# Optimization experiments

Hardware: AMD Instinct MI355X
Metric: run time of the kernel (lower is better)

Reference implementation:

```python
import jax, jax.numpy as jnp
import numpy as np

T, D, H, KEXP = 91, 256, 4, 4
DH = D // H
NA, NRG = 128, 1024
NEG = -1e10
SCALE = 2.0  # sqrt(head_num=4), faithful to the original (NOT sqrt(dh))


def _ln(x, g, b, eps=1e-5):
    m = jnp.mean(x, axis=-1, keepdims=True)
    v = jnp.mean((x - m) ** 2, axis=-1, keepdims=True)
    return (x - m) * jax.lax.rsqrt(v + eps) * g + b


def setup_inputs() -> dict:
    key = jax.random.key(0)
    ks = jax.random.split(key, 16)
    s = lambda fan_in: 1.0 / np.sqrt(fan_in)
    inp = {
        "agent": jax.random.normal(ks[0], (NA, T, D), jnp.float32),
        "rg": jax.random.normal(ks[1], (NRG, T, D), jnp.float32),
        "ln_x_g": jnp.ones((D,), jnp.float32),
        "ln_x_b": jnp.zeros((D,), jnp.float32),
        "wk": jax.random.uniform(ks[2], (D, D), jnp.float32, -s(D), s(D)),
        "bk": jnp.zeros((D,), jnp.float32),
        "wv": jax.random.uniform(ks[3], (D, D), jnp.float32, -s(D), s(D)),
        "bv": jnp.zeros((D,), jnp.float32),
        "wq": jax.random.uniform(ks[4], (D, D), jnp.float32, -s(D), s(D)),
        "bq": jnp.zeros((D,), jnp.float32),
        "q_scale": jnp.full((DH,), 0.001, jnp.float32),
        "wy": jax.random.uniform(ks[5], (D, D), jnp.float32, -s(D), s(D)),
        "by": jnp.zeros((D,), jnp.float32),
        "wf1": jax.random.uniform(ks[6], (D, KEXP * D), jnp.float32, -s(D), s(D)),
        "bf1": jnp.zeros((KEXP * D,), jnp.float32),
        "wf2": jax.random.uniform(ks[7], (KEXP * D, D), jnp.float32, -s(KEXP * D), s(KEXP * D)),
        "bf2": jnp.zeros((D,), jnp.float32),
        "ln_z_g": jnp.ones((D,), jnp.float32),
        "ln_z_b": jnp.zeros((D,), jnp.float32),
        "agent_rg_mask": jax.random.randint(ks[8], (T, NA, NRG), 0, 2).astype(bool),
        "padding_mask": jax.random.randint(ks[9], (T, NRG), 0, 2).astype(bool),
        "rg_valid_mask": jax.random.randint(ks[10], (T, NA), 0, 2).astype(bool),
    }
    return inp


def reference(agent, rg, ln_x_g, ln_x_b, wk, bk, wv, bv, wq, bq, q_scale,
              wy, by, wf1, bf1, wf2, bf2, ln_z_g, ln_z_b,
              agent_rg_mask, padding_mask, rg_valid_mask):
    agent_n = _ln(agent, ln_x_g, ln_x_b)   # (Na, T, D)
    rg_n = _ln(rg, ln_x_g, ln_x_b)         # (Nrg, T, D)

    K = jax.nn.relu(rg_n @ wk + bk).reshape(NRG, T, H, DH)
    V = jax.nn.relu(rg_n @ wv + bv).reshape(NRG, T, H, DH)
    Q = jax.nn.relu(agent_n @ wq + bq).reshape(NA, T, H, DH) * q_scale

    # energy: (T, H, Na, Nrg)
    energy = jnp.einsum("athd,rthd->thar", Q, K) / SCALE
    energy = jnp.where(agent_rg_mask[:, None, :, :], energy, NEG)
    energy = jnp.where(padding_mask[:, None, None, :], energy, NEG)
    energy = jnp.where(rg_valid_mask[:, None, :, None], energy, NEG)
    attn = jax.nn.softmax(energy, axis=-1)

    Y1 = jnp.einsum("thar,rthd->athd", attn, V).reshape(NA, T, D)
    Y2 = jax.nn.relu(Y1 @ wy + by)
    S = Y2 + agent_n
    F1 = jax.nn.relu(S @ wf1 + bf1)
    F2 = jax.nn.relu(F1 @ wf2 + bf2)
    Z = _ln(F2, ln_z_g, ln_z_b)

    Qp = jnp.transpose(Q, (1, 2, 0, 3))  # (T,H,Na,dh)
    Kp = jnp.transpose(K, (1, 2, 0, 3))
    Vp = jnp.transpose(V, (1, 2, 0, 3))
    return (Z, Qp, Kp, Vp)
```

## Files before the change

### kernel.cpp

```cpp
#include <hip/hip_runtime.h>

#define T_   91
#define D_   256
#define H_   4
#define DH_  64
#define NA_  128
#define NRG_ 1024
#define KEXP_ 4

typedef float f32x4 __attribute__((ext_vector_type(4)));
typedef short bf16x8 __attribute__((ext_vector_type(8)));

static constexpr float P_EPS = 1.3877787807814457e-17f;

__device__ inline ushort f2bf(float f) {
    union { float f; unsigned u; } v; v.f = f;
    unsigned r = (v.u + 0x7fffu + ((v.u >> 16) & 1u)) >> 16;
    return (ushort)r;
}
__device__ inline unsigned pk2(float a, float b) {
    return (unsigned)f2bf(a) | ((unsigned)f2bf(b) << 16);
}
__device__ inline float bf2f(ushort b) {
    union { unsigned u; float f; } v; v.u = ((unsigned)b) << 16;
    return v.f;
}

#define LN_BLOCKS 2912
#define PM_BLOCKS 2912
#define PW_BLOCKS 3072

__global__ __launch_bounds__(256) void prep_all(
    const float* __restrict__ agent,
    const float* __restrict__ g, const float* __restrict__ b,
    const int* __restrict__ am, const int* __restrict__ pm,
    const int* __restrict__ vmk,
    const float* __restrict__ wk, const float* __restrict__ wv,
    const float* __restrict__ wq, const float* __restrict__ wy,
    const float* __restrict__ wf1, const float* __restrict__ wf2,
    ushort* __restrict__ agn, unsigned* __restrict__ cm,
    ushort* __restrict__ wkvt, ushort* __restrict__ wqt,
    ushort* __restrict__ wyt, ushort* __restrict__ wf1t,
    ushort* __restrict__ wf2t) {
    __shared__ int pmS[NRG_];
    int bid = blockIdx.x;
    if (bid < LN_BLOCKS) {
        int row = bid * 4 + (threadIdx.x >> 6);
        int lane = threadIdx.x & 63;
        f32x4 x = *(const f32x4*)(agent + (size_t)row * D_ + lane * 4);
        float s1 = x[0] + x[1] + x[2] + x[3];
        float s2 = x[0] * x[0] + x[1] * x[1] + x[2] * x[2] + x[3] * x[3];
#pragma unroll
        for (int off = 1; off < 64; off <<= 1) {
            s1 += __shfl_xor(s1, off);
            s2 += __shfl_xor(s2, off);
        }
        float mean = s1 * (1.0f / 256.0f);
        float var = s2 * (1.0f / 256.0f) - mean * mean;
        float rstd = rsqrtf(var + 1e-5f);
        f32x4 gv = *(const f32x4*)(g + lane * 4);
        f32x4 bv = *(const f32x4*)(b + lane * 4);
        float y0 = (x[0] - mean) * rstd * gv[0] + bv[0];
        float y1 = (x[1] - mean) * rstd * gv[1] + bv[1];
        float y2 = (x[2] - mean) * rstd * gv[2] + bv[2];
        float y3 = (x[3] - mean) * rstd * gv[3] + bv[3];
        *(uint2*)(agn + (size_t)row * D_ + lane * 4) =
            make_uint2(pk2(y0, y1), pk2(y2, y3));
    } else if (bid < LN_BLOCKS + PM_BLOCKS) {
        int base = (bid - LN_BLOCKS) * 4;
        int t = base / NA_;
        int w = threadIdx.x >> 6, lane = threadIdx.x & 63;
#pragma unroll
        for (int i = 0; i < 4; ++i)
            pmS[threadIdx.x + i * 256] = pm[(size_t)t * NRG_ + threadIdx.x + i * 256];
        __syncthreads();
        int idx = base + w;
        int a = idx & (NA_ - 1);
        int valid = vmk[t * NA_ + a];
        const int* amrow = am + (size_t)idx * NRG_;
#pragma unroll
        for (int c = 0; c < 16; ++c) {
            int r = c * 64 + lane;
            bool bit = valid && amrow[r] && pmS[r];
            unsigned long long msk = __ballot(bit);
            if (lane == 0) {
                cm[(size_t)idx * 32 + c * 2]     = (unsigned)msk;
                cm[(size_t)idx * 32 + c * 2 + 1] = (unsigned)(msk >> 32);
            }
        }
    } else {
        int idx = (bid - LN_BLOCKS - PM_BLOCKS) * 256 + threadIdx.x;
        if (idx < 131072) {
            const float* W = (idx < 65536) ? wk : wv;
            int li = idx & 65535;
            int n = li >> 8, k = li & 255;
            wkvt[idx] = f2bf(W[(size_t)k * 256 + n]);
        } else if (idx < 196608) {
            int li = idx - 131072;
            int n = li >> 8, k = li & 255;
            wqt[li] = f2bf(wq[(size_t)k * 256 + n]);
        } else if (idx < 262144) {
            int li = idx - 196608;
            int n = li >> 8, k = li & 255;
            wyt[li] = f2bf(wy[(size_t)k * 256 + n]);
        } else if (idx < 524288) {
            int li = idx - 262144;
            int n = li >> 8, k = li & 255;
            wf1t[li] = f2bf(wf1[(size_t)k * 1024 + n]);
        } else {
            int li = idx - 524288;
            int n = li >> 10, k = li & 1023;
            wf2t[li] = f2bf(wf2[(size_t)k * 256 + n]);
        }
    }
}

__global__ __launch_bounds__(512) void gemm_kvq(
    const float* __restrict__ rgf, const ushort* __restrict__ agn,
    const float* __restrict__ lng, const float* __restrict__ lnb,
    const ushort* __restrict__ wkvt, const ushort* __restrict__ wqt,
    const float* __restrict__ bk, const float* __restrict__ bv,
    const float* __restrict__ bq, const float* __restrict__ qs,
    float* __restrict__ Kp, float* __restrict__ Vp, float* __restrict__ Qp,
    ushort* __restrict__ Kb, ushort* __restrict__ Vtb, ushort* __restrict__ Qb) {
    __shared__ ushort Asf[64][264];
    __shared__ ushort Bs[256][72];
    float (*Et)[68] = (float(*)[68])&Asf[0][0];

    int bid = blockIdx.x;
    bool isQ = bid >= 2912;
    int bxi = 0, t, rb = 0, a0 = 0, bn = 0;
    if (!isQ) {
        int sub = bid & 15, pid = bid >> 4;
        bxi = sub >> 3;
        int by = pid * 8 + (sub & 7);
        t = by >> 4; rb = (by & 15) << 6;
        bn = bxi << 8;
    } else {
        int qid = bid - 2912;
        t = qid >> 1; a0 = (qid & 1) << 6;
    }
    const ushort* Bt = isQ ? wqt : wkvt;

    int tid = threadIdx.x;
    int w = tid >> 6, lane = tid & 63;
    int wm = w >> 2, wn = w & 3;
    int l15 = lane & 15, l4 = lane >> 4;

    if (!isQ) {
        int row = tid >> 3, l8 = tid & 7;
        const float* ap = rgf + ((size_t)(rb + row) * T_ + t) * 256;
        f32x4 xr[8];
#pragma unroll
        for (int c = 0; c < 8; ++c) xr[c] = *(const f32x4*)(ap + l8 * 4 + c * 32);
        float s1 = 0.0f, s2 = 0.0f;
#pragma unroll
        for (int c = 0; c < 8; ++c)
#pragma unroll
            for (int r = 0; r < 4; ++r) { s1 += xr[c][r]; s2 += xr[c][r] * xr[c][r]; }
#pragma unroll
        for (int off = 1; off < 8; off <<= 1) {
            s1 += __shfl_xor(s1, off);
            s2 += __shfl_xor(s2, off);
        }
        float mean = s1 * (1.0f / 256.0f);
        float var = s2 * (1.0f / 256.0f) - mean * mean;
        float rstd = rsqrtf(var + 1e-5f);
#pragma unroll
        for (int c = 0; c < 8; ++c) {
            int col = l8 * 4 + c * 32;
            f32x4 g4 = *(const f32x4*)(lng + col);
            f32x4 b4 = *(const f32x4*)(lnb + col);
            float y0 = (xr[c][0] - mean) * rstd * g4[0] + b4[0];
            float y1 = (xr[c][1] - mean) * rstd * g4[1] + b4[1];
            float y2 = (xr[c][2] - mean) * rstd * g4[2] + b4[2];
            float y3 = (xr[c][3] - mean) * rstd * g4[3] + b4[3];
            *(uint2*)&Asf[row][col] = make_uint2(pk2(y0, y1), pk2(y2, y3));
        }
    } else {
#pragma unroll
        for (int i2 = 0; i2 < 4; ++i2) {
            int chunk = tid + i2 * 512;
            int row = chunk >> 5, c8 = (chunk & 31) * 8;
            *(bf16x8*)&Asf[row][c8] =
                *(const bf16x8*)(agn + ((size_t)(a0 + row) * T_ + t) * 256 + c8);
        }
    }

    f32x4 acc[2][4];
#pragma unroll
    for (int i = 0; i < 2; ++i)
#pragma unroll
        for (int j = 0; j < 4; ++j)
#pragma unroll
            for (int r = 0; r < 4; ++r) acc[i][j][r] = 0.0f;

    for (int k0 = 0; k0 < 256; k0 += 64) {
#pragma unroll
        for (int it = 0; it < 4; ++it) {
            int li = tid + it * 512;
            int row = li >> 3, c8 = (li & 7) * 8;
            *(bf16x8*)&Bs[row][c8] =
                *(const bf16x8*)(Bt + (size_t)(bn + row) * 256 + k0 + c8);
        }
        __syncthreads();
#pragma unroll
        for (int kk = 0; kk < 2; ++kk) {
            bf16x8 af[2], bfr[4];
#pragma unroll
            for (int i = 0; i < 2; ++i)
                af[i] = *(const bf16x8*)&Asf[wm * 32 + i * 16 + l15][k0 + kk * 32 + l4 * 8];
#pragma unroll
            for (int j = 0; j < 4; ++j)
                bfr[j] = *(const bf16x8*)&Bs[wn * 64 + j * 16 + l15][kk * 32 + l4 * 8];
#pragma unroll
            for (int i = 0; i < 2; ++i)
#pragma unroll
                for (int j = 0; j < 4; ++j)
                    acc[i][j] = __builtin_amdgcn_mfma_f32_16x16x32_bf16(
                        af[i], bfr[j], acc[i][j], 0, 0, 0);
        }
        __syncthreads();
    }

    float v[2][4][4];
#pragma unroll
    for (int i = 0; i < 2; ++i)
#pragma unroll
        for (int j = 0; j < 4; ++j)
#pragma unroll
            for (int reg = 0; reg < 4; ++reg) {
                int nl = wn * 64 + j * 16 + l15;
                float bs = isQ ? bq[nl] : (bxi ? bv[nl] : bk[nl]);
                float x = fmaxf(acc[i][j][reg] + bs, 0.0f);
                if (isQ) x *= qs[nl & 63];
                v[i][j][reg] = x;
            }

#pragma unroll 1
    for (int jq = 0; jq < 4; ++jq) {
        __syncthreads();
        if (wn == jq) {
#pragma unroll
            for (int i = 0; i < 2; ++i)
#pragma unroll
                for (int j = 0; j < 4; ++j)
#pragma unroll
                    for (int reg = 0; reg < 4; ++reg)
                        Et[wm * 32 + i * 16 + l4 * 4 + reg][j * 16 + l15] = v[i][j][reg];
        }
        __syncthreads();

        if (isQ) {
            size_t base = (((size_t)t * H_ + jq) * NA_ + a0) * DH_;
#pragma unroll
            for (int it = 0; it < 2; ++it) {
                int slot = it * 512 + tid;
                int row = slot >> 4, c4 = (slot & 15) * 4;
                *(f32x4*)(Qp + base + row * 64 + c4) = *(f32x4*)&Et[row][c4];
                uint2 u = make_uint2(pk2(Et[row][c4] * 0.5f, Et[row][c4 + 1] * 0.5f),
                                     pk2(Et[row][c4 + 2] * 0.5f, Et[row][c4 + 3] * 0.5f));
                *(uint2*)(Qb + base + row * 64 + c4) = u;
            }
        } else {
            size_t base = (((size_t)t * H_ + jq) * NRG_ + rb) * DH_;
            float* of = bxi ? Vp : Kp;
#pragma unroll
            for (int it = 0; it < 2; ++it) {
                int slot = it * 512 + tid;
                int row = slot >> 4, c4 = (slot & 15) * 4;
                *(f32x4*)(of + base + row * 64 + c4) = *(f32x4*)&Et[row][c4];
            }
            if (!bxi) {
#pragma unroll
                for (int it = 0; it < 2; ++it) {
                    int slot = it * 512 + tid;
                    int row = slot >> 4, c4 = (slot & 15) * 4;
                    uint2 u = make_uint2(pk2(Et[row][c4], Et[row][c4 + 1]),
                                         pk2(Et[row][c4 + 2], Et[row][c4 + 3]));
                    *(uint2*)(Kb + base + row * 64 + c4) = u;
                }
            } else {
                __syncthreads();
                if (wn == jq) {
#pragma unroll
                    for (int i = 0; i < 2; ++i)
#pragma unroll
                        for (int j = 0; j < 4; ++j)
#pragma unroll
                            for (int reg = 0; reg < 4; ++reg)
                                Et[j * 16 + l15][wm * 32 + i * 16 + l4 * 4 + reg] = v[i][j][reg];
                }
                __syncthreads();
                size_t tb = ((size_t)t * H_ + jq) * DH_ * NRG_;
#pragma unroll
                for (int it = 0; it < 2; ++it) {
                    int slot = it * 512 + tid;
                    int d = slot >> 4, r4 = (slot & 15) * 4;
                    uint2 u = make_uint2(pk2(Et[d][r4], Et[d][r4 + 1]),
                                         pk2(Et[d][r4 + 2], Et[d][r4 + 3]));
                    *(uint2*)(Vtb + tb + (size_t)d * NRG_ + rb + r4) = u;
                }
            }
        }
    }
}

__global__ __launch_bounds__(512) void gemm_wide(
    const ushort* __restrict__ Ab, const ushort* __restrict__ Bt,
    const float* __restrict__ bias0, const float* __restrict__ bias1,
    const float* __restrict__ aux0, const ushort* __restrict__ residb,
    float* __restrict__ out0, ushort* __restrict__ out2,
    int N, int K, int mode) {
    __shared__ ushort smem[64 * 72 + 256 * 72];
    __shared__ float lnp[2][64][4];
    ushort (*As)[72] = (ushort(*)[72])smem;
    ushort (*Bs)[72] = (ushort(*)[72])(smem + 64 * 72);
    float (*Et)[68] = (float(*)[68])smem;

    int bxi = blockIdx.x, by = blockIdx.y;
    int bn = bxi * 256, bm = by * 64;

    int tid = threadIdx.x;
    int w = tid >> 6, lane = tid & 63;
    int wm = w >> 2, wn = w & 3;
    int l15 = lane & 15, l4 = lane >> 4;

    f32x4 acc[2][4];
#pragma unroll
    for (int i = 0; i < 2; ++i)
#pragma unroll
        for (int j = 0; j < 4; ++j)
#pragma unroll
            for (int r = 0; r < 4; ++r) acc[i][j][r] = 0.0f;

    for (int k0 = 0; k0 < K; k0 += 64) {
        {
            int row = tid >> 3, c8 = (tid & 7) * 8;
            *(bf16x8*)&As[row][c8] =
                *(const bf16x8*)(Ab + (size_t)(bm + row) * K + k0 + c8);
        }
#pragma unroll
        for (int it = 0; it < 4; ++it) {
            int li = tid + it * 512;
            int row = li >> 3, c8 = (li & 7) * 8;
            *(bf16x8*)&Bs[row][c8] =
                *(const bf16x8*)(Bt + (size_t)(bn + row) * K + k0 + c8);
        }
        __syncthreads();
#pragma unroll
        for (int kk = 0; kk < 2; ++kk) {
            bf16x8 af[2], bfr[4];
#pragma unroll
            for (int i = 0; i < 2; ++i)
                af[i] = *(const bf16x8*)&As[wm * 32 + i * 16 + l15][kk * 32 + l4 * 8];
#pragma unroll
            for (int j = 0; j < 4; ++j)
                bfr[j] = *(const bf16x8*)&Bs[wn * 64 + j * 16 + l15][kk * 32 + l4 * 8];
#pragma unroll
            for (int i = 0; i < 2; ++i)
#pragma unroll
                for (int j = 0; j < 4; ++j)
                    acc[i][j] = __builtin_amdgcn_mfma_f32_16x16x32_bf16(
                        af[i], bfr[j], acc[i][j], 0, 0, 0);
        }
        __syncthreads();
    }

    float v[2][4][4];
#pragma unroll
    for (int i = 0; i < 2; ++i)
#pragma unroll
        for (int j = 0; j < 4; ++j)
#pragma unroll
            for (int reg = 0; reg < 4; ++reg) {
                int nl = wn * 64 + j * 16 + l15;
                int rowl = wm * 32 + i * 16 + l4 * 4 + reg;
                float bs = (mode == 0) ? bias0[bn + nl] : bias0[nl];
                float x = fmaxf(acc[i][j][reg] + bs, 0.0f);
                if (mode == 3) x += bf2f(residb[(size_t)(bm + rowl) * 256 + nl]);
                v[i][j][reg] = x;
            }

    if (mode == 5) {
        float rs_[2][4], rq_[2][4];
#pragma unroll
        for (int i = 0; i < 2; ++i)
#pragma unroll
            for (int reg = 0; reg < 4; ++reg) {
                float s = 0.0f, q = 0.0f;
#pragma unroll
                for (int j = 0; j < 4; ++j) {
                    float x = v[i][j][reg];
                    s += x; q += x * x;
                }
#pragma unroll
                for (int off = 1; off < 16; off <<= 1) {
                    s += __shfl_xor(s, off);
                    q += __shfl_xor(q, off);
                }
                rs_[i][reg] = s; rq_[i][reg] = q;
            }
        if (l15 == 0) {
#pragma unroll
            for (int i = 0; i < 2; ++i)
#pragma unroll
                for (int reg = 0; reg < 4; ++reg) {
                    int row = wm * 32 + i * 16 + l4 * 4 + reg;
                    lnp[0][row][wn] = rs_[i][reg];
                    lnp[1][row][wn] = rq_[i][reg];
                }
        }
        __syncthreads();
#pragma unroll
        for (int i = 0; i < 2; ++i)
#pragma unroll
            for (int reg = 0; reg < 4; ++reg) {
                int row = wm * 32 + i * 16 + l4 * 4 + reg;
                float S1 = lnp[0][row][0] + lnp[0][row][1] + lnp[0][row][2] + lnp[0][row][3];
                float S2 = lnp[1][row][0] + lnp[1][row][1] + lnp[1][row][2] + lnp[1][row][3];
                float mean = S1 * (1.0f / 256.0f);
                float var = S2 * (1.0f / 256.0f) - mean * mean;
                float rstd = rsqrtf(var + 1e-5f);
#pragma unroll
                for (int j = 0; j < 4; ++j) {
                    int nl = wn * 64 + j * 16 + l15;
                    float z = (v[i][j][reg] - mean) * rstd * bias1[nl] + aux0[nl];
                    out0[(size_t)(bm + row) * 256 + nl] = z;
                }
            }
        return;
    }

#pragma unroll 1
    for (int jq = 0; jq < 4; ++jq) {
        __syncthreads();
        if (wn == jq) {
#pragma unroll
            for (int i = 0; i < 2; ++i)
#pragma unroll
                for (int j = 0; j < 4; ++j)
#pragma unroll
                    for (int reg = 0; reg < 4; ++reg)
                        Et[wm * 32 + i * 16 + l4 * 4 + reg][j * 16 + l15] = v[i][j][reg];
        }
        __syncthreads();
#pragma unroll
        for (int it = 0; it < 2; ++it) {
            int slot = it * 512 + tid;
            int row = slot >> 4, c4 = (slot & 15) * 4;
            uint2 u = make_uint2(pk2(Et[row][c4], Et[row][c4 + 1]),
                                 pk2(Et[row][c4 + 2], Et[row][c4 + 3]));
            *(uint2*)(out2 + (size_t)(bm + row) * N + bn + jq * 64 + c4) = u;
        }
    }
}

__global__ __launch_bounds__(512) void attn_flash(
    const ushort* __restrict__ Qb, const ushort* __restrict__ Kb,
    const ushort* __restrict__ Vtb, const unsigned* __restrict__ cm,
    ushort* __restrict__ Y1b) {
    int th = blockIdx.x;
    int t = th >> 2, h = th & 3;
    int tid = threadIdx.x;
    int w = tid >> 6, lane = tid & 63;
    int l15 = lane & 15, l4 = lane >> 4;

    __shared__ ushort Ks[2][64][72];
    __shared__ ushort Vts[2][64][72];
    __shared__ ushort Ps[128][72];
    __shared__ unsigned cmAll[128][33];

    bf16x8 qf[2];
#pragma unroll
    for (int kk = 0; kk < 2; ++kk)
        qf[kk] = *(const bf16x8*)(Qb + ((size_t)th * NA_ + w * 16 + l15) * DH_
                                  + kk * 32 + l4 * 8);

    {
        const uint4* src = (const uint4*)(cm + (size_t)t * NA_ * 32 + tid * 8);
        uint4 c0 = src[0], c1 = src[1];
        int a = tid >> 2, wd = (tid & 3) * 8;
        cmAll[a][wd + 0] = c0.x; cmAll[a][wd + 1] = c0.y;
        cmAll[a][wd + 2] = c0.z; cmAll[a][wd + 3] = c0.w;
        cmAll[a][wd + 4] = c1.x; cmAll[a][wd + 5] = c1.y;
        cmAll[a][wd + 6] = c1.z; cmAll[a][wd + 7] = c1.w;
    }

    int srow = tid >> 3, sc8 = (tid & 7) * 8;
    const ushort* Kbase = Kb + (size_t)th * NRG_ * DH_;
    const ushort* Vbase = Vtb + (size_t)th * DH_ * NRG_;
    bf16x8 kreg = *(const bf16x8*)(Kbase + (size_t)srow * DH_ + sc8);
    bf16x8 vreg = *(const bf16x8*)(Vbase + (size_t)srow * NRG_ + sc8);
    *(bf16x8*)&Ks[0][srow][sc8] = kreg;
    *(bf16x8*)&Vts[0][srow][sc8] = vreg;
    __syncthreads();

    f32x4 o[4];
    float rsum[4] = {0.0f, 0.0f, 0.0f, 0.0f};
#pragma unroll
    for (int ds = 0; ds < 4; ++ds)
#pragma unroll
        for (int r = 0; r < 4; ++r) o[ds][r] = 0.0f;

    for (int rt = 0; rt < 16; ++rt) {
        int cur = rt & 1;
        if (rt < 15) {
            int r0n = (rt + 1) * 64;
            kreg = *(const bf16x8*)(Kbase + (size_t)(r0n + srow) * DH_ + sc8);
            vreg = *(const bf16x8*)(Vbase + (size_t)srow * NRG_ + r0n + sc8);
        }

        f32x4 e[4];
#pragma unroll
        for (int rs = 0; rs < 4; ++rs) {
#pragma unroll
            for (int r = 0; r < 4; ++r) e[rs][r] = 0.0f;
#pragma unroll
            for (int kk = 0; kk < 2; ++kk) {
                bf16x8 kf = *(const bf16x8*)&Ks[cur][rs * 16 + l15][kk * 32 + l4 * 8];
                e[rs] = __builtin_amdgcn_mfma_f32_16x16x32_bf16(qf[kk], kf, e[rs], 0, 0, 0);
            }
        }

#pragma unroll
        for (int reg = 0; reg < 4; ++reg) {
            int a_loc = w * 16 + l4 * 4 + reg;
            unsigned w0 = cmAll[a_loc][rt * 2], w1 = cmAll[a_loc][rt * 2 + 1];
#pragma unroll
            for (int rs = 0; rs < 4; ++rs) {
                unsigned wd = (rs & 2) ? w1 : w0;
                int bit = (wd >> ((rs & 1) * 16 + l15)) & 1;
                float p = bit ? __expf(e[rs][reg]) : P_EPS;
                rsum[reg] += p;
                Ps[a_loc][rs * 16 + l15] = f2bf(p);
            }
        }

#pragma unroll
        for (int rc = 0; rc < 2; ++rc) {
            bf16x8 pa = *(const bf16x8*)&Ps[w * 16 + l15][rc * 32 + l4 * 8];
#pragma unroll
            for (int ds = 0; ds < 4; ++ds) {
                bf16x8 vf = *(const bf16x8*)&Vts[cur][ds * 16 + l15][rc * 32 + l4 * 8];
                o[ds] = __builtin_amdgcn_mfma_f32_16x16x32_bf16(pa, vf, o[ds], 0, 0, 0);
            }
        }

        if (rt < 15) {
            *(bf16x8*)&Ks[cur ^ 1][srow][sc8] = kreg;
            *(bf16x8*)&Vts[cur ^ 1][srow][sc8] = vreg;
            __syncthreads();
        }
    }

#pragma unroll
    for (int off = 1; off < 16; off <<= 1)
#pragma unroll
        for (int reg = 0; reg < 4; ++reg)
            rsum[reg] += __shfl_xor(rsum[reg], off);
    float rinv[4];
#pragma unroll
    for (int reg = 0; reg < 4; ++reg) rinv[reg] = 1.0f / rsum[reg];

#pragma unroll
    for (int ds = 0; ds < 4; ++ds)
#pragma unroll
        for (int reg = 0; reg < 4; ++reg) {
            int a_g = w * 16 + l4 * 4 + reg;
            int d = ds * 16 + l15;
            Y1b[((size_t)a_g * T_ + t) * D_ + h * DH_ + d] = f2bf(o[ds][reg] * rinv[reg]);
        }
}

extern "C" void kernel_launch(void* const* d_in, const int* in_sizes, int n_in,
                              void* d_out, int out_size, void* d_ws, size_t ws_size,
                              hipStream_t stream) {
    const float* agent   = (const float*)d_in[0];
    const float* rg      = (const float*)d_in[1];
    const float* ln_x_g  = (const float*)d_in[2];
    const float* ln_x_b  = (const float*)d_in[3];
    const float* wk      = (const float*)d_in[4];
    const float* bk      = (const float*)d_in[5];
    const float* wv      = (const float*)d_in[6];
    const float* bv      = (const float*)d_in[7];
    const float* wq      = (const float*)d_in[8];
    const float* bq      = (const float*)d_in[9];
    const float* q_scale = (const float*)d_in[10];
    const float* wy      = (const float*)d_in[11];
    const float* by      = (const float*)d_in[12];
    const float* wf1     = (const float*)d_in[13];
    const float* bf1     = (const float*)d_in[14];
    const float* wf2     = (const float*)d_in[15];
    const float* bf2     = (const float*)d_in[16];
    const float* ln_z_g  = (const float*)d_in[17];
    const float* ln_z_b  = (const float*)d_in[18];
    const int*   am      = (const int*)d_in[19];
    const int*   pm      = (const int*)d_in[20];
    const int*   vmk     = (const int*)d_in[21];

    float* Z  = (float*)d_out;
    float* Qp = Z + (size_t)NA_ * T_ * D_;
    float* Kp = Qp + (size_t)NA_ * T_ * D_;
    float* Vp = Kp + (size_t)NRG_ * T_ * D_;

    char* p = (char*)d_ws;
    ushort* agn_b = (ushort*)p;   p += (size_t)NA_ * T_ * D_ * 2;
    ushort* wkvt  = (ushort*)p;   p += (size_t)512 * 256 * 2;
    ushort* wqt   = (ushort*)p;   p += (size_t)256 * 256 * 2;
    ushort* wyt   = (ushort*)p;   p += (size_t)256 * 256 * 2;
    ushort* wf1t  = (ushort*)p;   p += (size_t)1024 * 256 * 2;
    ushort* wf2t  = (ushort*)p;   p += (size_t)256 * 1024 * 2;
    unsigned* cm  = (unsigned*)p; p += (size_t)T_ * NA_ * 32 * 4;
    ushort* Kb    = (ushort*)p;   p += (size_t)T_ * H_ * NRG_ * DH_ * 2;
    ushort* Vtb   = (ushort*)p;   p += (size_t)T_ * H_ * NRG_ * DH_ * 2;
    ushort* Qb    = (ushort*)p;   p += (size_t)T_ * H_ * NA_ * DH_ * 2;
    ushort* Y1b   = (ushort*)p;   p += (size_t)NA_ * T_ * D_ * 2;
    ushort* Sb    = (ushort*)p;   p += (size_t)NA_ * T_ * D_ * 2;
    ushort* F1b   = (ushort*)p;   p += (size_t)NA_ * T_ * D_ * KEXP_ * 2;

    prep_all<<<dim3(LN_BLOCKS + PM_BLOCKS + PW_BLOCKS), dim3(256), 0, stream>>>(
        agent, ln_x_g, ln_x_b, am, pm, vmk,
        wk, wv, wq, wy, wf1, wf2,
        agn_b, cm, wkvt, wqt, wyt, wf1t, wf2t);

    gemm_kvq<<<dim3(2912 + T_ * 2), dim3(512), 0, stream>>>(
        rg, agn_b, ln_x_g, ln_x_b, wkvt, wqt, bk, bv, bq, q_scale,
        Kp, Vp, Qp, Kb, Vtb, Qb);

    attn_flash<<<dim3(T_ * H_), dim3(512), 0, stream>>>(Qb, Kb, Vtb, cm, Y1b);

    gemm_wide<<<dim3(1, NA_ * T_ / 64), dim3(512), 0, stream>>>(
        Y1b, wyt, by, nullptr, nullptr, agn_b,
        nullptr, Sb, 256, 256, 3);

    gemm_wide<<<dim3(4, NA_ * T_ / 64), dim3(512), 0, stream>>>(
        Sb, wf1t, bf1, nullptr, nullptr, nullptr,
        nullptr, F1b, 1024, 256, 0);

    gemm_wide<<<dim3(1, NA_ * T_ / 64), dim3(512), 0, stream>>>(
        F1b, wf2t, bf2, ln_z_g, ln_z_b, nullptr,
        Z, nullptr, 256, 1024, 5);
}
```

Baseline: 245.7 us.

## Halve gemm_kvq N-tile to 128 columns, doubling block count for occupancy

Each KV/Q projection block now computes a 64x128 output tile (two heads) instead of 64x256, so the grid doubles and the B shared tile and accumulators shrink. This lowers per-block LDS and register use, which should raise occupancy and spread work across more CUs. In exchange, each block re-reads rg and recomputes its layernorm twice as often, and the V-transpose epilogue is moved into a separate loop after the K/V writes.

```diff
diff --git a/kernel.cpp b/kernel.cpp
--- a/kernel.cpp
+++ b/kernel.cpp
@@ -29,6 +29,7 @@
 #define LN_BLOCKS 2912
 #define PM_BLOCKS 2912
 #define PW_BLOCKS 3072
+#define KV_BLOCKS 5824
 
 __global__ __launch_bounds__(256) void prep_all(
     const float* __restrict__ agent,
@@ -124,23 +125,26 @@
     float* __restrict__ Kp, float* __restrict__ Vp, float* __restrict__ Qp,
     ushort* __restrict__ Kb, ushort* __restrict__ Vtb, ushort* __restrict__ Qb) {
     __shared__ ushort Asf[64][264];
-    __shared__ ushort Bs[256][72];
+    __shared__ ushort Bs[128][72];
     float (*Et)[68] = (float(*)[68])&Asf[0][0];
 
     int bid = blockIdx.x;
-    bool isQ = bid >= 2912;
-    int bxi = 0, t, rb = 0, a0 = 0, bn = 0;
+    bool isQ = bid >= KV_BLOCKS;
+    int bxi = 0, nh, t, rb = 0, a0 = 0;
     if (!isQ) {
-        int sub = bid & 15, pid = bid >> 4;
-        bxi = sub >> 3;
-        int by = pid * 8 + (sub & 7);
-        t = by >> 4; rb = (by & 15) << 6;
-        bn = bxi << 8;
+        int chunk = bid >> 5, rem = bid & 31;
+        int q = rem >> 3;
+        int tidx = chunk * 8 + (rem & 7);
+        bxi = q >> 1; nh = q & 1;
+        t = tidx >> 4; rb = (tidx & 15) << 6;
     } else {
-        int qid = bid - 2912;
-        t = qid >> 1; a0 = (qid & 1) << 6;
-    }
-    const ushort* Bt = isQ ? wqt : wkvt;
+        int qid = bid - KV_BLOCKS;
+        t = qid >> 2;
+        int sub = qid & 3;
+        a0 = (sub >> 1) << 6; nh = sub & 1;
+    }
+    int bnw = bxi * 256 + nh * 128;
+    const ushort* Bt = isQ ? (wqt + (size_t)nh * 128 * 256) : (wkvt + (size_t)bnw * 256);
 
     int tid = threadIdx.x;
     int w = tid >> 6, lane = tid & 63;
@@ -187,72 +191,75 @@
         }
     }
 
-    f32x4 acc[2][4];
+    f32x4 acc[2][2];
 #pragma unroll
     for (int i = 0; i < 2; ++i)
 #pragma unroll
-        for (int j = 0; j < 4; ++j)
+        for (int j = 0; j < 2; ++j)
 #pragma unroll
             for (int r = 0; r < 4; ++r) acc[i][j][r] = 0.0f;
 
     for (int k0 = 0; k0 < 256; k0 += 64) {
 #pragma unroll
-        for (int it = 0; it < 4; ++it) {
+        for (int it = 0; it < 2; ++it) {
             int li = tid + it * 512;
             int row = li >> 3, c8 = (li & 7) * 8;
             *(bf16x8*)&Bs[row][c8] =
-                *(const bf16x8*)(Bt + (size_t)(bn + row) * 256 + k0 + c8);
+                *(const bf16x8*)(Bt + (size_t)row * 256 + k0 + c8);
         }
         __syncthreads();
 #pragma unroll
         for (int kk = 0; kk < 2; ++kk) {
-            bf16x8 af[2], bfr[4];
+            bf16x8 af[2], bfr[2];
 #pragma unroll
             for (int i = 0; i < 2; ++i)
                 af[i] = *(const bf16x8*)&Asf[wm * 32 + i * 16 + l15][k0 + kk * 32 + l4 * 8];
 #pragma unroll
-            for (int j = 0; j < 4; ++j)
-                bfr[j] = *(const bf16x8*)&Bs[wn * 64 + j * 16 + l15][kk * 32 + l4 * 8];
+            for (int j = 0; j < 2; ++j)
+                bfr[j] = *(const bf16x8*)&Bs[wn * 32 + j * 16 + l15][kk * 32 + l4 * 8];
 #pragma unroll
             for (int i = 0; i < 2; ++i)
 #pragma unroll
-                for (int j = 0; j < 4; ++j)
+                for (int j = 0; j < 2; ++j)
                     acc[i][j] = __builtin_amdgcn_mfma_f32_16x16x32_bf16(
                         af[i], bfr[j], acc[i][j], 0, 0, 0);
         }
         __syncthreads();
     }
 
-    float v[2][4][4];
+    float v[2][2][4];
 #pragma unroll
     for (int i = 0; i < 2; ++i)
 #pragma unroll
-        for (int j = 0; j < 4; ++j)
+        for (int j = 0; j < 2; ++j)
 #pragma unroll
             for (int reg = 0; reg < 4; ++reg) {
-                int nl = wn * 64 + j * 16 + l15;
-                float bs = isQ ? bq[nl] : (bxi ? bv[nl] : bk[nl]);
+                int nl = wn * 32 + j * 16 + l15;
+                int np = nh * 128 + nl;
+                float bs = isQ ? bq[np] : (bxi ? bv[np] : bk[np]);
                 float x = fmaxf(acc[i][j][reg] + bs, 0.0f);
-                if (isQ) x *= qs[nl & 63];
+                if (isQ) x *= qs[np & 63];
                 v[i][j][reg] = x;
             }
 
 #pragma unroll 1
-    for (int jq = 0; jq < 4; ++jq) {
-        __syncthreads();
-        if (wn == jq) {
+    for (int jq = 0; jq < 2; ++jq) {
+        __syncthreads();
+        if ((wn >> 1) == jq) {
 #pragma unroll
             for (int i = 0; i < 2; ++i)
 #pragma unroll
-                for (int j = 0; j < 4; ++j)
+                for (int j = 0; j < 2; ++j)
 #pragma unroll
                     for (int reg = 0; reg < 4; ++reg)
-                        Et[wm * 32 + i * 16 + l4 * 4 + reg][j * 16 + l15] = v[i][j][reg];
-        }
-        __syncthreads();
+                        Et[wm * 32 + i * 16 + l4 * 4 + reg][(wn & 1) * 32 + j * 16 + l15]
+                            = v[i][j][reg];
+        }
+        __syncthreads();
+        int h = nh * 2 + jq;
 
         if (isQ) {
-            size_t base = (((size_t)t * H_ + jq) * NA_ + a0) * DH_;
+            size_t base = (((size_t)t * H_ + h) * NA_ + a0) * DH_;
 #pragma unroll
             for (int it = 0; it < 2; ++it) {
                 int slot = it * 512 + tid;
@@ -263,7 +270,7 @@
                 *(uint2*)(Qb + base + row * 64 + c4) = u;
             }
         } else {
-            size_t base = (((size_t)t * H_ + jq) * NRG_ + rb) * DH_;
+            size_t base = (((size_t)t * H_ + h) * NRG_ + rb) * DH_;
             float* of = bxi ? Vp : Kp;
 #pragma unroll
             for (int it = 0; it < 2; ++it) {
@@ -280,27 +287,34 @@
                                          pk2(Et[row][c4 + 2], Et[row][c4 + 3]));
                     *(uint2*)(Kb + base + row * 64 + c4) = u;
                 }
-            } else {
-                __syncthreads();
-                if (wn == jq) {
-#pragma unroll
-                    for (int i = 0; i < 2; ++i)
-#pragma unroll
-                        for (int j = 0; j < 4; ++j)
-#pragma unroll
-                            for (int reg = 0; reg < 4; ++reg)
-                                Et[j * 16 + l15][wm * 32 + i * 16 + l4 * 4 + reg] = v[i][j][reg];
-                }
-                __syncthreads();
-                size_t tb = ((size_t)t * H_ + jq) * DH_ * NRG_;
-#pragma unroll
-                for (int it = 0; it < 2; ++it) {
-                    int slot = it * 512 + tid;
-                    int d = slot >> 4, r4 = (slot & 15) * 4;
-                    uint2 u = make_uint2(pk2(Et[d][r4], Et[d][r4 + 1]),
-                                         pk2(Et[d][r4 + 2], Et[d][r4 + 3]));
-                    *(uint2*)(Vtb + tb + (size_t)d * NRG_ + rb + r4) = u;
-                }
+            }
+        }
+    }
+
+    if (!isQ && bxi) {
+#pragma unroll 1
+        for (int jq = 0; jq < 2; ++jq) {
+            __syncthreads();
+            if ((wn >> 1) == jq) {
+#pragma unroll
+                for (int i = 0; i < 2; ++i)
+#pragma unroll
+                    for (int j = 0; j < 2; ++j)
+#pragma unroll
+                        for (int reg = 0; reg < 4; ++reg)
+                            Et[(wn & 1) * 32 + j * 16 + l15]
+                              [wm * 32 + i * 16 + l4 * 4 + reg] = v[i][j][reg];
+            }
+            __syncthreads();
+            int h = nh * 2 + jq;
+            size_t tb = ((size_t)t * H_ + h) * DH_ * NRG_;
+#pragma unroll
+            for (int it = 0; it < 2; ++it) {
+                int slot = it * 512 + tid;
+                int d = slot >> 4, r4 = (slot & 15) * 4;
+                uint2 u = make_uint2(pk2(Et[d][r4], Et[d][r4 + 1]),
+                                     pk2(Et[d][r4 + 2], Et[d][r4 + 3]));
+                *(uint2*)(Vtb + tb + (size_t)d * NRG_ + rb + r4) = u;
             }
         }
     }
@@ -624,7 +638,7 @@
         wk, wv, wq, wy, wf1, wf2,
         agn_b, cm, wkvt, wqt, wyt, wf1t, wf2t);
 
-    gemm_kvq<<<dim3(2912 + T_ * 2), dim3(512), 0, stream>>>(
+    gemm_kvq<<<dim3(KV_BLOCKS + T_ * 4), dim3(512), 0, stream>>>(
         rg, agn_b, ln_x_g, ln_x_b, wkvt, wqt, bk, bv, bq, q_scale,
         Kp, Vp, Qp, Kb, Vtb, Qb);
 
```

After: 252.8 us. 1.03x slower.
